# Optimization experiments

Hardware: AMD Instinct MI355X
Metric: run time of the kernel (lower is better)

Reference implementation:

```python
import jax, jax.numpy as jnp
import numpy as np

HEADS = 4
C = 128            # per-head out channels (hard-coded 128 in the module)
NEG_SLOPE_ATT = 0.2   # GATConv attention leaky_relu slope
NEG_SLOPE = 0.01      # F.leaky_relu default slope


def _diag_output_ids(num_groups, n):
    # ids = base_i + n*j + j for group i, agent j; base_i = i * n^2
    i = np.arange(num_groups)[:, None] * (n * n)
    j = np.arange(n)[None, :] * (n + 1)
    return jnp.asarray((i + j).reshape(-1))


def setup_inputs() -> dict:
    key = jax.random.key(0)
    ks = jax.random.split(key, 12)
    num_groups, n_agents = 12, 48
    N = num_groups * n_agents * n_agents      # 27648 nodes
    E = 442368
    F_in, edge_dim, hidden = 256, 16, 256
    s = 0.05
    return {
        "x": jax.random.normal(ks[0], (N, F_in), jnp.float32),
        "edge_index": jax.random.randint(ks[1], (2, E), 0, N, jnp.int32),
        "edge_attr": jax.random.normal(ks[2], (E, edge_dim), jnp.float32),
        "num_groups": num_groups,
        "agents_per_group": n_agents,
        "W": jax.random.normal(ks[3], (F_in, HEADS * C), jnp.float32) * s,
        "att_src": jax.random.normal(ks[4], (HEADS, C), jnp.float32) * s,
        "att_dst": jax.random.normal(ks[5], (HEADS, C), jnp.float32) * s,
        "W_edge": jax.random.normal(ks[6], (edge_dim, HEADS * C), jnp.float32) * s,
        "att_edge": jax.random.normal(ks[7], (HEADS, C), jnp.float32) * s,
        "bias_gat": jnp.zeros((HEADS * C,), jnp.float32),
        "fc_W": jax.random.normal(ks[8], (HEADS * C, hidden), jnp.float32) * s,
        "fc_b": jnp.zeros((hidden,), jnp.float32),
    }


def _gat_conv(x, src, dst, edge_attr_full, W, att_src, att_dst, W_edge, att_edge, bias):
    N = x.shape[0]
    h = (x @ W).reshape(N, HEADS, C)                       # [N,H,C]
    a_src = jnp.einsum('nhc,hc->nh', h, att_src)           # [N,H]
    a_dst = jnp.einsum('nhc,hc->nh', h, att_dst)
    he = (edge_attr_full @ W_edge).reshape(-1, HEADS, C)   # [E',H,C]
    a_edge = jnp.einsum('ehc,hc->eh', he, att_edge)
    logits = jax.nn.leaky_relu(a_src[src] + a_dst[dst] + a_edge, NEG_SLOPE_ATT)
    # segment softmax over incoming edges of each dst node
    m = jax.ops.segment_max(logits, dst, num_segments=N)   # [N,H]
    e = jnp.exp(logits - m[dst])
    s = jax.ops.segment_sum(e, dst, num_segments=N)
    alpha = e / (s[dst] + 1e-16)                           # [E',H]
    msg = h[src] * alpha[..., None]                        # [E',H,C]
    out = jax.ops.segment_sum(msg, dst, num_segments=N)    # [N,H,C]
    return out.reshape(N, HEADS * C) + bias


def reference(x, edge_index, edge_attr, num_groups, agents_per_group,
              W, att_src, att_dst, W_edge, att_edge, bias_gat, fc_W, fc_b):
    N = x.shape[0]
    # add self-loops (PyG default), self-loop edge_attr = mean fill
    loops = jnp.arange(N, dtype=edge_index.dtype)
    src = jnp.concatenate([edge_index[0], loops])
    dst = jnp.concatenate([edge_index[1], loops])
    ea = jnp.concatenate([edge_attr,
                          jnp.broadcast_to(edge_attr.mean(0), (N, edge_attr.shape[1]))])
    h = jax.nn.leaky_relu(
        _gat_conv(x, src, dst, ea, W, att_src, att_dst, W_edge, att_edge, bias_gat),
        NEG_SLOPE)
    ids = _diag_output_ids(num_groups, agents_per_group)
    # fc_output + leaky_relu then diagonal index-select (select first: same math)
    return jax.nn.leaky_relu(h[ids] @ fc_W + fc_b, NEG_SLOPE)
```

## Files before the change

kernel.cpp:

```cpp
#include <hip/hip_runtime.h>

#define NNODES 27648
#define NEDGES 442368
#define FIN    256
#define HC     512
#define NH     4
#define CDIM   128
#define NAG    48
#define NGRP   12
#define N2     2304
#define NOUT   576
#define CAP    128
#define EDIM   16
#define NBUCK  32

__device__ __forceinline__ float lrelu(float v, float s){ return v > 0.0f ? v : s * v; }

__device__ __forceinline__ float wsum(float v){
  #pragma unroll
  for (int off = 32; off; off >>= 1) v += __shfl_xor(v, off, 64);
  return v;
}
__device__ __forceinline__ float wmax(float v){
  #pragma unroll
  for (int off = 32; off; off >>= 1) v = fmaxf(v, __shfl_xor(v, off, 64));
  return v;
}

__global__ __launch_bounds__(256) void k_prescan(
    const float* __restrict__ W, const float* __restrict__ att_src,
    const float* __restrict__ att_dst, const float* __restrict__ W_edge,
    const float* __restrict__ att_edge,
    const int* __restrict__ ei, const float* __restrict__ ea,
    float* __restrict__ ws_, float* __restrict__ wd_, float* __restrict__ we_,
    float* __restrict__ easum32, int* __restrict__ counts,
    int2* __restrict__ slist2){
  __shared__ float4 red[16];
  int b = blockIdx.x, tid = threadIdx.x;
  if (b < NEDGES/256){
    int e = b*256 + tid;
    int dst = ei[NEDGES + e];
    int r = dst % N2;
    if (r % 49 == 0){
      int row = (dst / N2) * NAG + r / 49;
      int pos = atomicAdd(&counts[row], 1);
      if (pos < CAP) slist2[row*CAP + pos] = make_int2(ei[e], e);
    }
    const float4* p4 = (const float4*)ea + (size_t)b*1024;
    float4 acc = p4[tid];
    float4 v1 = p4[tid+256], v2 = p4[tid+512], v3 = p4[tid+768];
    acc.x += v1.x+v2.x+v3.x; acc.y += v1.y+v2.y+v3.y;
    acc.z += v1.z+v2.z+v3.z; acc.w += v1.w+v2.w+v3.w;
    #pragma unroll
    for (int off = 4; off <= 32; off <<= 1){
      acc.x += __shfl_xor(acc.x, off, 64);
      acc.y += __shfl_xor(acc.y, off, 64);
      acc.z += __shfl_xor(acc.z, off, 64);
      acc.w += __shfl_xor(acc.w, off, 64);
    }
    int lane = tid & 63, wave = tid >> 6;
    if (lane < 4) red[wave*4 + lane] = acc;
    __syncthreads();
    if (tid < 4){
      float4 t = red[tid], u = red[4+tid], v = red[8+tid], w = red[12+tid];
      t.x += u.x+v.x+w.x; t.y += u.y+v.y+w.y;
      t.z += u.z+v.z+w.z; t.w += u.w+v.w+w.w;
      float* dp = easum32 + (b & (NBUCK-1))*16 + tid*4;
      atomicAdd(dp+0, t.x); atomicAdd(dp+1, t.y);
      atomicAdd(dp+2, t.z); atomicAdd(dp+3, t.w);
    }
  } else {
    int g = (b - NEDGES/256)*256 + tid;
    if (g < 1024) {
      int f = g >> 2, h = g & 3;
      const float4* wp = (const float4*)(W + f*HC + h*CDIM);
      const float4* ap = (const float4*)(att_src + h*CDIM);
      float s = 0.f;
      #pragma unroll 8
      for (int c4 = 0; c4 < CDIM/4; c4++){
        float4 wv = wp[c4], av = ap[c4];
        s += wv.x*av.x + wv.y*av.y + wv.z*av.z + wv.w*av.w;
      }
      ws_[g] = s;
    } else if (g < 2048) {
      int gg = g - 1024; int f = gg >> 2, h = gg & 3;
      const float4* wp = (const float4*)(W + f*HC + h*CDIM);
      const float4* ap = (const float4*)(att_dst + h*CDIM);
      float s = 0.f;
      #pragma unroll 8
      for (int c4 = 0; c4 < CDIM/4; c4++){
        float4 wv = wp[c4], av = ap[c4];
        s += wv.x*av.x + wv.y*av.y + wv.z*av.z + wv.w*av.w;
      }
      wd_[gg] = s;
    } else if (g < 2112) {
      int gg = g - 2048; int d = gg >> 2, h = gg & 3;
      const float4* wp = (const float4*)(W_edge + d*HC + h*CDIM);
      const float4* ap = (const float4*)(att_edge + h*CDIM);
      float s = 0.f;
      #pragma unroll 8
      for (int c4 = 0; c4 < CDIM/4; c4++){
        float4 wv = wp[c4], av = ap[c4];
        s += wv.x*av.x + wv.y*av.y + wv.z*av.z + wv.w*av.w;
      }
      we_[gg] = s;
    }
  }
}

__global__ __launch_bounds__(256) void k_attn(const float* __restrict__ x,
    const float* __restrict__ ws_, const float* __restrict__ wd_,
    const float* __restrict__ we_, const float* __restrict__ easum32,
    const int* __restrict__ counts, const int2* __restrict__ slist2,
    const float* __restrict__ ea, float* __restrict__ z){
  __shared__ float lg[(CAP+1)*4];
  __shared__ int   srcs[CAP];
  __shared__ float adst_s[4];
  int row = blockIdx.x;
  int g = row / NAG, j = row - g*NAG;
  int dst = g*N2 + j*49;
  int tid = threadIdx.x;
  int lane = tid & 63, wave = tid >> 6;
  int k = counts[row]; if (k > CAP) k = CAP;

  float4 wev = make_float4(0.f, 0.f, 0.f, 0.f);
  if (lane < 16) wev = *(const float4*)(we_ + lane*4);

  float wsr[4][4];
  #pragma unroll
  for (int q = 0; q < 4; q++){
    float4 t = *(const float4*)(ws_ + (lane*4+q)*4);
    wsr[q][0]=t.x; wsr[q][1]=t.y; wsr[q][2]=t.z; wsr[q][3]=t.w;
  }

  for (int i = wave; i < k; i += 4){
    int2 se = slist2[row*CAP + i];
    float eav = (lane < 16) ? ea[(size_t)se.y*EDIM + lane] : 0.f;
    float4 xv = *(const float4*)(x + (size_t)se.x*FIN + lane*4);
    float p0 = xv.x*wsr[0][0] + xv.y*wsr[1][0] + xv.z*wsr[2][0] + xv.w*wsr[3][0] + eav*wev.x;
    float p1 = xv.x*wsr[0][1] + xv.y*wsr[1][1] + xv.z*wsr[2][1] + xv.w*wsr[3][1] + eav*wev.y;
    float p2 = xv.x*wsr[0][2] + xv.y*wsr[1][2] + xv.z*wsr[2][2] + xv.w*wsr[3][2] + eav*wev.z;
    float p3 = xv.x*wsr[0][3] + xv.y*wsr[1][3] + xv.z*wsr[2][3] + xv.w*wsr[3][3] + eav*wev.w;
    p0 = wsum(p0); p1 = wsum(p1); p2 = wsum(p2); p3 = wsum(p3);
    if (lane == 0){
      srcs[i] = se.x;
      lg[i*4+0] = p0; lg[i*4+1] = p1; lg[i*4+2] = p2; lg[i*4+3] = p3;
    }
  }

  if (wave == 0){
    float wdr[4][4];
    #pragma unroll
    for (int q = 0; q < 4; q++){
      float4 t = *(const float4*)(wd_ + (lane*4+q)*4);
      wdr[q][0]=t.x; wdr[q][1]=t.y; wdr[q][2]=t.z; wdr[q][3]=t.w;
    }
    float4 xv = *(const float4*)(x + (size_t)dst*FIN + lane*4);
    float pd[4], ps[4];
    #pragma unroll
    for (int h = 0; h < 4; h++){
      pd[h] = xv.x*wdr[0][h] + xv.y*wdr[1][h] + xv.z*wdr[2][h] + xv.w*wdr[3][h];
      ps[h] = xv.x*wsr[0][h] + xv.y*wsr[1][h] + xv.z*wsr[2][h] + xv.w*wsr[3][h];
    }
    float s = 0.f;
    if (lane < 16){
      #pragma unroll
      for (int bb = 0; bb < NBUCK; bb++) s += easum32[bb*16 + lane];
    }
    float md = s * (1.0f/(float)NEDGES);
    float al[4];
    al[0] = wsum(md*wev.x); al[1] = wsum(md*wev.y);
    al[2] = wsum(md*wev.z); al[3] = wsum(md*wev.w);
    #pragma unroll
    for (int h = 0; h < 4; h++){ pd[h] = wsum(pd[h]); ps[h] = wsum(ps[h]); }
    if (lane == 0){
      #pragma unroll
      for (int h = 0; h < 4; h++){
        adst_s[h] = pd[h];
        lg[k*4+h] = ps[h] + al[h];
      }
    }
  }
  __syncthreads();

  {
    int h = wave;
    float ad = adst_s[h];
    float m = -1e30f;
    for (int i = lane; i <= k; i += 64){
      float v = lrelu(lg[i*4+h] + ad, 0.2f);
      lg[i*4+h] = v;
      m = fmaxf(m, v);
    }
    m = wmax(m);
    float s = 0.f;
    for (int i = lane; i <= k; i += 64){
      float e = __expf(lg[i*4+h] - m);
      lg[i*4+h] = e;
      s += e;
    }
    s = wsum(s);
    float inv = 1.0f/(s + 1e-16f);
    for (int i = lane; i <= k; i += 64) lg[i*4+h] *= inv;
  }
  __syncthreads();

  int f = tid;
  float a0=0.f,a1=0.f,a2=0.f,a3=0.f;
  for (int i = 0; i < k; i++){
    float xv = x[(size_t)srcs[i]*FIN + f];
    a0 += lg[i*4+0]*xv; a1 += lg[i*4+1]*xv; a2 += lg[i*4+2]*xv; a3 += lg[i*4+3]*xv;
  }
  {
    float xv = x[(size_t)dst*FIN + f];
    a0 += lg[k*4+0]*xv; a1 += lg[k*4+1]*xv; a2 += lg[k*4+2]*xv; a3 += lg[k*4+3]*xv;
  }
  float* zp = z + (size_t)row*1024;
  zp[0*256+f]=a0; zp[1*256+f]=a1; zp[2*256+f]=a2; zp[3*256+f]=a3;
}

__global__ __launch_bounds__(256) void k_mlp(const float* __restrict__ z,
    const float* __restrict__ W, const float* __restrict__ bias,
    const float* __restrict__ fcW, const float* __restrict__ fcb,
    float* __restrict__ out){
  __shared__ float zs[4*1024];
  __shared__ float hs[4*512];
  int base = blockIdx.x * 4;
  int tid = threadIdx.x;
  {
    const float4* sp = (const float4*)(z + (size_t)base*1024);
    float4* dp = (float4*)zs;
    #pragma unroll
    for (int i = 0; i < 4; i++) dp[tid + i*256] = sp[tid + i*256];
  }
  __syncthreads();
  {
    int h = tid >> 6, c = tid & 63;
    int o0 = h*CDIM + c, o1 = o0 + 64;
    float a0[4] = {0,0,0,0}, a1[4] = {0,0,0,0};
    for (int k0 = 0; k0 < 256; k0 += 4){
      float w00 = W[(size_t)(k0+0)*HC + o0], w10 = W[(size_t)(k0+0)*HC + o1];
      float w01 = W[(size_t)(k0+1)*HC + o0], w11 = W[(size_t)(k0+1)*HC + o1];
      float w02 = W[(size_t)(k0+2)*HC + o0], w12 = W[(size_t)(k0+2)*HC + o1];
      float w03 = W[(size_t)(k0+3)*HC + o0], w13 = W[(size_t)(k0+3)*HC + o1];
      #pragma unroll
      for (int r = 0; r < 4; r++){
        float4 zv = *(const float4*)&zs[r*1024 + h*256 + k0];
        a0[r] += zv.x*w00 + zv.y*w01 + zv.z*w02 + zv.w*w03;
        a1[r] += zv.x*w10 + zv.y*w11 + zv.z*w12 + zv.w*w13;
      }
    }
    float b0 = bias[o0], b1 = bias[o1];
    #pragma unroll
    for (int r = 0; r < 4; r++){
      hs[r*HC + o0] = lrelu(a0[r] + b0, 0.01f);
      hs[r*HC + o1] = lrelu(a1[r] + b1, 0.01f);
    }
  }
  __syncthreads();
  {
    int j = tid;
    float acc[4] = {0,0,0,0};
    for (int q0 = 0; q0 < 512; q0 += 4){
      float f0 = fcW[(size_t)(q0+0)*256 + j];
      float f1 = fcW[(size_t)(q0+1)*256 + j];
      float f2 = fcW[(size_t)(q0+2)*256 + j];
      float f3 = fcW[(size_t)(q0+3)*256 + j];
      #pragma unroll
      for (int r = 0; r < 4; r++){
        float4 hv = *(const float4*)&hs[r*HC + q0];
        acc[r] += hv.x*f0 + hv.y*f1 + hv.z*f2 + hv.w*f3;
      }
    }
    float bj = fcb[j];
    #pragma unroll
    for (int r = 0; r < 4; r++)
      out[(size_t)(base+r)*256 + j] = lrelu(acc[r] + bj, 0.01f);
  }
}

extern "C" void kernel_launch(void* const* d_in, const int* in_sizes, int n_in,
                              void* d_out, int out_size, void* d_ws, size_t ws_size,
                              hipStream_t stream) {
  const float* x        = (const float*)d_in[0];
  const int*   ei       = (const int*)  d_in[1];
  const float* ea       = (const float*)d_in[2];
  const float* W        = (const float*)d_in[5];
  const float* att_src  = (const float*)d_in[6];
  const float* att_dst  = (const float*)d_in[7];
  const float* W_edge   = (const float*)d_in[8];
  const float* att_edge = (const float*)d_in[9];
  const float* bias     = (const float*)d_in[10];
  const float* fcW      = (const float*)d_in[11];
  const float* fcb      = (const float*)d_in[12];
  float* out = (float*)d_out;

  float* w = (float*)d_ws;
  float* ws_     = w;
  float* wd_     = w + 1024;
  float* we_     = w + 2048;
  float* easum32 = w + 2112;
  int*   counts  = (int*)(w + 2624);
  int2*  slist2  = (int2*)(w + 3200);
  float* z       = w + 150656;

  hipMemsetAsync(w + 2112, 0, (512 + 576) * sizeof(float), stream);
  k_prescan<<<NEDGES/256 + 11, 256, 0, stream>>>(
      W, att_src, att_dst, W_edge, att_edge, ei, ea,
      ws_, wd_, we_, easum32, counts, slist2);
  k_attn<<<NOUT, 256, 0, stream>>>(x, ws_, wd_, we_, easum32, counts, slist2, ea, z);
  k_mlp<<<144, 256, 0, stream>>>(z, W, bias, fcW, fcb, out);
}
```

Baseline: 166.8 us.

## Fuse prescan, attention and MLP into one cooperative persistent kernel

Replaces the memset plus three kernel launches with a single cooperative kernel of 512 blocks that runs the three phases in grid-stride loops, separated by grid-wide syncs. The goal is to remove per-launch overhead and the gaps between kernels on a workload that is short overall. The cost is grid.sync barriers, and phases that use only part of the grid (576 rows over 512 blocks, 144 MLP blocks) leave the rest idle. If the cooperative launch fails, the code falls back to the old three-kernel path.

Measured after the change: 343.5 us. +106.0%, slower.

```diff
diff --git a/kernel.cpp b/kernel.cpp
--- a/kernel.cpp
+++ b/kernel.cpp
@@ -1,4 +1,7 @@
 #include <hip/hip_runtime.h>
+#include <hip/hip_cooperative_groups.h>
+
+namespace cg = cooperative_groups;
 
 #define NNODES 27648
 #define NEDGES 442368
@@ -13,6 +16,7 @@
 #define CAP    128
 #define EDIM   16
 #define NBUCK  32
+#define GRID   512
 
 __device__ __forceinline__ float lrelu(float v, float s){ return v > 0.0f ? v : s * v; }
 
@@ -25,6 +29,244 @@
   #pragma unroll
   for (int off = 32; off; off >>= 1) v = fmaxf(v, __shfl_xor(v, off, 64));
   return v;
+}
+
+__global__ __launch_bounds__(256, 2) void k_fused(
+    const float* __restrict__ x, const int* __restrict__ ei,
+    const float* __restrict__ ea, const float* __restrict__ W,
+    const float* __restrict__ att_src, const float* __restrict__ att_dst,
+    const float* __restrict__ W_edge, const float* __restrict__ att_edge,
+    const float* __restrict__ bias, const float* __restrict__ fcW,
+    const float* __restrict__ fcb,
+    float* __restrict__ ws_, float* __restrict__ wd_, float* __restrict__ we_,
+    float* __restrict__ easum32, int* __restrict__ counts,
+    int2* __restrict__ slist2, float* __restrict__ z, float* __restrict__ out){
+  cg::grid_group grid = cg::this_grid();
+  __shared__ __align__(16) float smem[6144];
+  int b = blockIdx.x, tid = threadIdx.x;
+  int lane = tid & 63, wave = tid >> 6;
+
+  if (b == 0){
+    for (int i = tid; i < 512; i += 256) easum32[i] = 0.f;
+    for (int i = tid; i < NOUT; i += 256) counts[i] = 0;
+  }
+  grid.sync();
+
+  for (int chunk = b; chunk < 1739; chunk += GRID){
+    if (chunk < NEDGES/256){
+      int e = chunk*256 + tid;
+      int dst = ei[NEDGES + e];
+      int r = dst % N2;
+      if (r % 49 == 0){
+        int row = (dst / N2) * NAG + r / 49;
+        int pos = atomicAdd(&counts[row], 1);
+        if (pos < CAP) slist2[row*CAP + pos] = make_int2(ei[e], e);
+      }
+      const float4* p4 = (const float4*)ea + (size_t)chunk*1024;
+      float4 acc = p4[tid];
+      float4 v1 = p4[tid+256], v2 = p4[tid+512], v3 = p4[tid+768];
+      acc.x += v1.x+v2.x+v3.x; acc.y += v1.y+v2.y+v3.y;
+      acc.z += v1.z+v2.z+v3.z; acc.w += v1.w+v2.w+v3.w;
+      #pragma unroll
+      for (int off = 4; off <= 32; off <<= 1){
+        acc.x += __shfl_xor(acc.x, off, 64);
+        acc.y += __shfl_xor(acc.y, off, 64);
+        acc.z += __shfl_xor(acc.z, off, 64);
+        acc.w += __shfl_xor(acc.w, off, 64);
+      }
+      float4* red = (float4*)smem;
+      if (lane < 4) red[wave*4 + lane] = acc;
+      __syncthreads();
+      if (tid < 4){
+        float4 t = red[tid], u = red[4+tid], v = red[8+tid], w4 = red[12+tid];
+        t.x += u.x+v.x+w4.x; t.y += u.y+v.y+w4.y;
+        t.z += u.z+v.z+w4.z; t.w += u.w+v.w+w4.w;
+        float* dp = easum32 + (chunk & (NBUCK-1))*16 + tid*4;
+        atomicAdd(dp+0, t.x); atomicAdd(dp+1, t.y);
+        atomicAdd(dp+2, t.z); atomicAdd(dp+3, t.w);
+      }
+      __syncthreads();
+    } else {
+      int g = (chunk - NEDGES/256)*256 + tid;
+      const float* wmat; const float* avec; float* dstp; int gg;
+      if (g < 1024)      { gg = g;        wmat = W + (gg>>2)*HC;      avec = att_src  + (gg&3)*CDIM; dstp = ws_ + gg; }
+      else if (g < 2048) { gg = g - 1024; wmat = W + (gg>>2)*HC;      avec = att_dst  + (gg&3)*CDIM; dstp = wd_ + gg; }
+      else if (g < 2112) { gg = g - 2048; wmat = W_edge + (gg>>2)*HC; avec = att_edge + (gg&3)*CDIM; dstp = we_ + gg; }
+      else continue;
+      const float4* wp = (const float4*)(wmat + (gg&3)*CDIM);
+      const float4* ap = (const float4*)avec;
+      float s = 0.f;
+      #pragma unroll 8
+      for (int c4 = 0; c4 < CDIM/4; c4++){
+        float4 wv = wp[c4], av = ap[c4];
+        s += wv.x*av.x + wv.y*av.y + wv.z*av.z + wv.w*av.w;
+      }
+      *dstp = s;
+    }
+  }
+  grid.sync();
+
+  for (int row = b; row < NOUT; row += GRID){
+    float* lg   = smem;
+    float* adst = smem + 516;
+    int*  srcs  = (int*)(smem + 520);
+    int g = row / NAG, j = row - g*NAG;
+    int dst = g*N2 + j*49;
+    int k = counts[row]; if (k > CAP) k = CAP;
+
+    float4 wev = make_float4(0.f, 0.f, 0.f, 0.f);
+    if (lane < 16) wev = *(const float4*)(we_ + lane*4);
+
+    float wsr[4][4];
+    #pragma unroll
+    for (int q = 0; q < 4; q++){
+      float4 t = *(const float4*)(ws_ + (lane*4+q)*4);
+      wsr[q][0]=t.x; wsr[q][1]=t.y; wsr[q][2]=t.z; wsr[q][3]=t.w;
+    }
+
+    for (int i = wave; i < k; i += 4){
+      int2 se = slist2[row*CAP + i];
+      float eav = (lane < 16) ? ea[(size_t)se.y*EDIM + lane] : 0.f;
+      float4 xv = *(const float4*)(x + (size_t)se.x*FIN + lane*4);
+      float p0 = xv.x*wsr[0][0] + xv.y*wsr[1][0] + xv.z*wsr[2][0] + xv.w*wsr[3][0] + eav*wev.x;
+      float p1 = xv.x*wsr[0][1] + xv.y*wsr[1][1] + xv.z*wsr[2][1] + xv.w*wsr[3][1] + eav*wev.y;
+      float p2 = xv.x*wsr[0][2] + xv.y*wsr[1][2] + xv.z*wsr[2][2] + xv.w*wsr[3][2] + eav*wev.z;
+      float p3 = xv.x*wsr[0][3] + xv.y*wsr[1][3] + xv.z*wsr[2][3] + xv.w*wsr[3][3] + eav*wev.w;
+      p0 = wsum(p0); p1 = wsum(p1); p2 = wsum(p2); p3 = wsum(p3);
+      if (lane == 0){
+        srcs[i] = se.x;
+        lg[i*4+0] = p0; lg[i*4+1] = p1; lg[i*4+2] = p2; lg[i*4+3] = p3;
+      }
+    }
+
+    if (wave == 0){
+      float wdr[4][4];
+      #pragma unroll
+      for (int q = 0; q < 4; q++){
+        float4 t = *(const float4*)(wd_ + (lane*4+q)*4);
+        wdr[q][0]=t.x; wdr[q][1]=t.y; wdr[q][2]=t.z; wdr[q][3]=t.w;
+      }
+      float4 xv = *(const float4*)(x + (size_t)dst*FIN + lane*4);
+      float pd[4], ps[4];
+      #pragma unroll
+      for (int h = 0; h < 4; h++){
+        pd[h] = xv.x*wdr[0][h] + xv.y*wdr[1][h] + xv.z*wdr[2][h] + xv.w*wdr[3][h];
+        ps[h] = xv.x*wsr[0][h] + xv.y*wsr[1][h] + xv.z*wsr[2][h] + xv.w*wsr[3][h];
+      }
+      float s = 0.f;
+      if (lane < 16){
+        #pragma unroll
+        for (int bb = 0; bb < NBUCK; bb++) s += easum32[bb*16 + lane];
+      }
+      float md = s * (1.0f/(float)NEDGES);
+      float al[4];
+      al[0] = wsum(md*wev.x); al[1] = wsum(md*wev.y);
+      al[2] = wsum(md*wev.z); al[3] = wsum(md*wev.w);
+      #pragma unroll
+      for (int h = 0; h < 4; h++){ pd[h] = wsum(pd[h]); ps[h] = wsum(ps[h]); }
+      if (lane == 0){
+        #pragma unroll
+        for (int h = 0; h < 4; h++){
+          adst[h] = pd[h];
+          lg[k*4+h] = ps[h] + al[h];
+        }
+      }
+    }
+    __syncthreads();
+
+    {
+      int h = wave;
+      float ad = adst[h];
+      float m = -1e30f;
+      for (int i = lane; i <= k; i += 64){
+        float v = lrelu(lg[i*4+h] + ad, 0.2f);
+        lg[i*4+h] = v;
+        m = fmaxf(m, v);
+      }
+      m = wmax(m);
+      float s = 0.f;
+      for (int i = lane; i <= k; i += 64){
+        float e = __expf(lg[i*4+h] - m);
+        lg[i*4+h] = e;
+        s += e;
+      }
+      s = wsum(s);
+      float inv = 1.0f/(s + 1e-16f);
+      for (int i = lane; i <= k; i += 64) lg[i*4+h] *= inv;
+    }
+    __syncthreads();
+
+    int f = tid;
+    float a0=0.f,a1=0.f,a2=0.f,a3=0.f;
+    for (int i = 0; i < k; i++){
+      float xv = x[(size_t)srcs[i]*FIN + f];
+      a0 += lg[i*4+0]*xv; a1 += lg[i*4+1]*xv; a2 += lg[i*4+2]*xv; a3 += lg[i*4+3]*xv;
+    }
+    {
+      float xv = x[(size_t)dst*FIN + f];
+      a0 += lg[k*4+0]*xv; a1 += lg[k*4+1]*xv; a2 += lg[k*4+2]*xv; a3 += lg[k*4+3]*xv;
+    }
+    float* zp = z + (size_t)row*1024;
+    zp[0*256+f]=a0; zp[1*256+f]=a1; zp[2*256+f]=a2; zp[3*256+f]=a3;
+    __syncthreads();
+  }
+  grid.sync();
+
+  if (b < 144){
+    float* zs = smem;
+    float* hs = smem + 4096;
+    int base = b * 4;
+    {
+      const float4* sp = (const float4*)(z + (size_t)base*1024);
+      float4* dp = (float4*)zs;
+      #pragma unroll
+      for (int i = 0; i < 4; i++) dp[tid + i*256] = sp[tid + i*256];
+    }
+    __syncthreads();
+    {
+      int h = wave, c = lane;
+      int o0 = h*CDIM + c, o1 = o0 + 64;
+      float a0[4] = {0,0,0,0}, a1[4] = {0,0,0,0};
+      for (int k0 = 0; k0 < 256; k0 += 4){
+        float w00 = W[(size_t)(k0+0)*HC + o0], w10 = W[(size_t)(k0+0)*HC + o1];
+        float w01 = W[(size_t)(k0+1)*HC + o0], w11 = W[(size_t)(k0+1)*HC + o1];
+        float w02 = W[(size_t)(k0+2)*HC + o0], w12 = W[(size_t)(k0+2)*HC + o1];
+        float w03 = W[(size_t)(k0+3)*HC + o0], w13 = W[(size_t)(k0+3)*HC + o1];
+        #pragma unroll
+        for (int r = 0; r < 4; r++){
+          float4 zv = *(const float4*)&zs[r*1024 + h*256 + k0];
+          a0[r] += zv.x*w00 + zv.y*w01 + zv.z*w02 + zv.w*w03;
+          a1[r] += zv.x*w10 + zv.y*w11 + zv.z*w12 + zv.w*w13;
+        }
+      }
+      float b0 = bias[o0], b1 = bias[o1];
+      #pragma unroll
+      for (int r = 0; r < 4; r++){
+        hs[r*HC + o0] = lrelu(a0[r] + b0, 0.01f);
+        hs[r*HC + o1] = lrelu(a1[r] + b1, 0.01f);
+      }
+    }
+    __syncthreads();
+    {
+      int j = tid;
+      float acc[4] = {0,0,0,0};
+      for (int q0 = 0; q0 < 512; q0 += 4){
+        float f0 = fcW[(size_t)(q0+0)*256 + j];
+        float f1 = fcW[(size_t)(q0+1)*256 + j];
+        float f2 = fcW[(size_t)(q0+2)*256 + j];
+        float f3 = fcW[(size_t)(q0+3)*256 + j];
+        #pragma unroll
+        for (int r = 0; r < 4; r++){
+          float4 hv = *(const float4*)&hs[r*HC + q0];
+          acc[r] += hv.x*f0 + hv.y*f1 + hv.z*f2 + hv.w*f3;
+        }
+      }
+      float bj = fcb[j];
+      #pragma unroll
+      for (int r = 0; r < 4; r++)
+        out[(size_t)(base+r)*256 + j] = lrelu(acc[r] + bj, 0.01f);
+    }
+  }
 }
 
 __global__ __launch_bounds__(256) void k_prescan(
@@ -62,49 +304,29 @@
     if (lane < 4) red[wave*4 + lane] = acc;
     __syncthreads();
     if (tid < 4){
-      float4 t = red[tid], u = red[4+tid], v = red[8+tid], w = red[12+tid];
-      t.x += u.x+v.x+w.x; t.y += u.y+v.y+w.y;
-      t.z += u.z+v.z+w.z; t.w += u.w+v.w+w.w;
+      float4 t = red[tid], u = red[4+tid], v = red[8+tid], w4 = red[12+tid];
+      t.x += u.x+v.x+w4.x; t.y += u.y+v.y+w4.y;
+      t.z += u.z+v.z+w4.z; t.w += u.w+v.w+w4.w;
       float* dp = easum32 + (b & (NBUCK-1))*16 + tid*4;
       atomicAdd(dp+0, t.x); atomicAdd(dp+1, t.y);
       atomicAdd(dp+2, t.z); atomicAdd(dp+3, t.w);
     }
   } else {
     int g = (b - NEDGES/256)*256 + tid;
-    if (g < 1024) {
-      int f = g >> 2, h = g & 3;
-      const float4* wp = (const float4*)(W + f*HC + h*CDIM);
-      const float4* ap = (const float4*)(att_src + h*CDIM);
-      float s = 0.f;
-      #pragma unroll 8
-      for (int c4 = 0; c4 < CDIM/4; c4++){
-        float4 wv = wp[c4], av = ap[c4];
-        s += wv.x*av.x + wv.y*av.y + wv.z*av.z + wv.w*av.w;
-      }
-      ws_[g] = s;
-    } else if (g < 2048) {
-      int gg = g - 1024; int f = gg >> 2, h = gg & 3;
-      const float4* wp = (const float4*)(W + f*HC + h*CDIM);
-      const float4* ap = (const float4*)(att_dst + h*CDIM);
-      float s = 0.f;
-      #pragma unroll 8
-      for (int c4 = 0; c4 < CDIM/4; c4++){
-        float4 wv = wp[c4], av = ap[c4];
-        s += wv.x*av.x + wv.y*av.y + wv.z*av.z + wv.w*av.w;
-      }
-      wd_[gg] = s;
-    } else if (g < 2112) {
-      int gg = g - 2048; int d = gg >> 2, h = gg & 3;
-      const float4* wp = (const float4*)(W_edge + d*HC + h*CDIM);
-      const float4* ap = (const float4*)(att_edge + h*CDIM);
-      float s = 0.f;
-      #pragma unroll 8
-      for (int c4 = 0; c4 < CDIM/4; c4++){
-        float4 wv = wp[c4], av = ap[c4];
-        s += wv.x*av.x + wv.y*av.y + wv.z*av.z + wv.w*av.w;
-      }
-      we_[gg] = s;
-    }
+    const float* wmat; const float* avec; float* dstp; int gg;
+    if (g < 1024)      { gg = g;        wmat = W + (gg>>2)*HC;      avec = att_src  + (gg&3)*CDIM; dstp = ws_ + gg; }
+    else if (g < 2048) { gg = g - 1024; wmat = W + (gg>>2)*HC;      avec = att_dst  + (gg&3)*CDIM; dstp = wd_ + gg; }
+    else if (g < 2112) { gg = g - 2048; wmat = W_edge + (gg>>2)*HC; avec = att_edge + (gg&3)*CDIM; dstp = we_ + gg; }
+    else return;
+    const float4* wp = (const float4*)(wmat + (gg&3)*CDIM);
+    const float4* ap = (const float4*)avec;
+    float s = 0.f;
+    #pragma unroll 8
+    for (int c4 = 0; c4 < CDIM/4; c4++){
+      float4 wv = wp[c4], av = ap[c4];
+      s += wv.x*av.x + wv.y*av.y + wv.z*av.z + wv.w*av.w;
+    }
+    *dstp = s;
   }
 }
 
@@ -304,10 +526,21 @@
   int2*  slist2  = (int2*)(w + 3200);
   float* z       = w + 150656;
 
-  hipMemsetAsync(w + 2112, 0, (512 + 576) * sizeof(float), stream);
-  k_prescan<<<NEDGES/256 + 11, 256, 0, stream>>>(
-      W, att_src, att_dst, W_edge, att_edge, ei, ea,
-      ws_, wd_, we_, easum32, counts, slist2);
-  k_attn<<<NOUT, 256, 0, stream>>>(x, ws_, wd_, we_, easum32, counts, slist2, ea, z);
-  k_mlp<<<144, 256, 0, stream>>>(z, W, bias, fcW, fcb, out);
-}
+  void* args[] = {
+    (void*)&x, (void*)&ei, (void*)&ea, (void*)&W, (void*)&att_src,
+    (void*)&att_dst, (void*)&W_edge, (void*)&att_edge, (void*)&bias,
+    (void*)&fcW, (void*)&fcb,
+    (void*)&ws_, (void*)&wd_, (void*)&we_, (void*)&easum32, (void*)&counts,
+    (void*)&slist2, (void*)&z, (void*)&out};
+  hipError_t err = hipLaunchCooperativeKernel((const void*)k_fused, dim3(GRID),
+                                              dim3(256), args, 0, stream);
+  if (err != hipSuccess){
+    (void)hipGetLastError();
+    hipMemsetAsync(w + 2112, 0, (512 + 576) * sizeof(float), stream);
+    k_prescan<<<NEDGES/256 + 11, 256, 0, stream>>>(
+        W, att_src, att_dst, W_edge, att_edge, ei, ea,
+        ws_, wd_, we_, easum32, counts, slist2);
+    k_attn<<<NOUT, 256, 0, stream>>>(x, ws_, wd_, we_, easum32, counts, slist2, ea, z);
+    k_mlp<<<144, 256, 0, stream>>>(z, W, bias, fcW, fcb, out);
+  }
+}
```

## Split attention aggregation across waves with float4 gathers and paired edge loads

Applied to the files above, without the earlier changes.

The weighted aggregation in k_attn now gives each wave a subset of edges, and every lane loads float4 slices of the source rows. Partial sums from the four waves are combined through a new 16KB shared buffer. The per-thread loop over all edges with scalar loads is gone. The logit loop and the aggregation loop both handle two edges per iteration to put more loads in flight. The self-loop node is appended to srcs, and the precompute branch is consolidated without changing its behavior. The extra shared memory and reduction add a barrier and may lower occupancy.

Measured after the change: 165.8 us. About the same (-0.6%).

```diff
diff --git a/kernel.cpp b/kernel.cpp
--- a/kernel.cpp
+++ b/kernel.cpp
@@ -62,49 +62,29 @@
     if (lane < 4) red[wave*4 + lane] = acc;
     __syncthreads();
     if (tid < 4){
-      float4 t = red[tid], u = red[4+tid], v = red[8+tid], w = red[12+tid];
-      t.x += u.x+v.x+w.x; t.y += u.y+v.y+w.y;
-      t.z += u.z+v.z+w.z; t.w += u.w+v.w+w.w;
+      float4 t = red[tid], u = red[4+tid], v = red[8+tid], w4 = red[12+tid];
+      t.x += u.x+v.x+w4.x; t.y += u.y+v.y+w4.y;
+      t.z += u.z+v.z+w4.z; t.w += u.w+v.w+w4.w;
       float* dp = easum32 + (b & (NBUCK-1))*16 + tid*4;
       atomicAdd(dp+0, t.x); atomicAdd(dp+1, t.y);
       atomicAdd(dp+2, t.z); atomicAdd(dp+3, t.w);
     }
   } else {
     int g = (b - NEDGES/256)*256 + tid;
-    if (g < 1024) {
-      int f = g >> 2, h = g & 3;
-      const float4* wp = (const float4*)(W + f*HC + h*CDIM);
-      const float4* ap = (const float4*)(att_src + h*CDIM);
-      float s = 0.f;
-      #pragma unroll 8
-      for (int c4 = 0; c4 < CDIM/4; c4++){
-        float4 wv = wp[c4], av = ap[c4];
-        s += wv.x*av.x + wv.y*av.y + wv.z*av.z + wv.w*av.w;
-      }
-      ws_[g] = s;
-    } else if (g < 2048) {
-      int gg = g - 1024; int f = gg >> 2, h = gg & 3;
-      const float4* wp = (const float4*)(W + f*HC + h*CDIM);
-      const float4* ap = (const float4*)(att_dst + h*CDIM);
-      float s = 0.f;
-      #pragma unroll 8
-      for (int c4 = 0; c4 < CDIM/4; c4++){
-        float4 wv = wp[c4], av = ap[c4];
-        s += wv.x*av.x + wv.y*av.y + wv.z*av.z + wv.w*av.w;
-      }
-      wd_[gg] = s;
-    } else if (g < 2112) {
-      int gg = g - 2048; int d = gg >> 2, h = gg & 3;
-      const float4* wp = (const float4*)(W_edge + d*HC + h*CDIM);
-      const float4* ap = (const float4*)(att_edge + h*CDIM);
-      float s = 0.f;
-      #pragma unroll 8
-      for (int c4 = 0; c4 < CDIM/4; c4++){
-        float4 wv = wp[c4], av = ap[c4];
-        s += wv.x*av.x + wv.y*av.y + wv.z*av.z + wv.w*av.w;
-      }
-      we_[gg] = s;
-    }
+    const float* wmat; const float* avec; float* dstp; int gg;
+    if (g < 1024)      { gg = g;        wmat = W + (gg>>2)*HC;      avec = att_src  + (gg&3)*CDIM; dstp = ws_ + gg; }
+    else if (g < 2048) { gg = g - 1024; wmat = W + (gg>>2)*HC;      avec = att_dst  + (gg&3)*CDIM; dstp = wd_ + gg; }
+    else if (g < 2112) { gg = g - 2048; wmat = W_edge + (gg>>2)*HC; avec = att_edge + (gg&3)*CDIM; dstp = we_ + gg; }
+    else return;
+    const float4* wp = (const float4*)(wmat + (gg&3)*CDIM);
+    const float4* ap = (const float4*)avec;
+    float s = 0.f;
+    #pragma unroll 8
+    for (int c4 = 0; c4 < CDIM/4; c4++){
+      float4 wv = wp[c4], av = ap[c4];
+      s += wv.x*av.x + wv.y*av.y + wv.z*av.z + wv.w*av.w;
+    }
+    *dstp = s;
   }
 }
 
@@ -114,8 +94,9 @@
     const int* __restrict__ counts, const int2* __restrict__ slist2,
     const float* __restrict__ ea, float* __restrict__ z){
   __shared__ float lg[(CAP+1)*4];
-  __shared__ int   srcs[CAP];
   __shared__ float adst_s[4];
+  __shared__ int   srcs[CAP+1];
+  __shared__ __align__(16) float zbuf[4][4][256];
   int row = blockIdx.x;
   int g = row / NAG, j = row - g*NAG;
   int dst = g*N2 + j*49;
@@ -133,18 +114,32 @@
     wsr[q][0]=t.x; wsr[q][1]=t.y; wsr[q][2]=t.z; wsr[q][3]=t.w;
   }
 
-  for (int i = wave; i < k; i += 4){
-    int2 se = slist2[row*CAP + i];
-    float eav = (lane < 16) ? ea[(size_t)se.y*EDIM + lane] : 0.f;
-    float4 xv = *(const float4*)(x + (size_t)se.x*FIN + lane*4);
-    float p0 = xv.x*wsr[0][0] + xv.y*wsr[1][0] + xv.z*wsr[2][0] + xv.w*wsr[3][0] + eav*wev.x;
-    float p1 = xv.x*wsr[0][1] + xv.y*wsr[1][1] + xv.z*wsr[2][1] + xv.w*wsr[3][1] + eav*wev.y;
-    float p2 = xv.x*wsr[0][2] + xv.y*wsr[1][2] + xv.z*wsr[2][2] + xv.w*wsr[3][2] + eav*wev.z;
-    float p3 = xv.x*wsr[0][3] + xv.y*wsr[1][3] + xv.z*wsr[2][3] + xv.w*wsr[3][3] + eav*wev.w;
-    p0 = wsum(p0); p1 = wsum(p1); p2 = wsum(p2); p3 = wsum(p3);
+  for (int i = wave; i < k; i += 8){
+    int iB = i + 4;
+    bool hasB = iB < k;
+    int2 seA = slist2[row*CAP + i];
+    int2 seB = hasB ? slist2[row*CAP + iB] : seA;
+    float eavA = (lane < 16) ? ea[(size_t)seA.y*EDIM + lane] : 0.f;
+    float eavB = (lane < 16) ? ea[(size_t)seB.y*EDIM + lane] : 0.f;
+    float4 xvA = *(const float4*)(x + (size_t)seA.x*FIN + lane*4);
+    float4 xvB = *(const float4*)(x + (size_t)seB.x*FIN + lane*4);
+    float pA[4], pB[4];
+    #pragma unroll
+    for (int h = 0; h < 4; h++){
+      pA[h] = xvA.x*wsr[0][h] + xvA.y*wsr[1][h] + xvA.z*wsr[2][h] + xvA.w*wsr[3][h];
+      pB[h] = xvB.x*wsr[0][h] + xvB.y*wsr[1][h] + xvB.z*wsr[2][h] + xvB.w*wsr[3][h];
+    }
+    pA[0] += eavA*wev.x; pA[1] += eavA*wev.y; pA[2] += eavA*wev.z; pA[3] += eavA*wev.w;
+    pB[0] += eavB*wev.x; pB[1] += eavB*wev.y; pB[2] += eavB*wev.z; pB[3] += eavB*wev.w;
+    #pragma unroll
+    for (int h = 0; h < 4; h++){ pA[h] = wsum(pA[h]); pB[h] = wsum(pB[h]); }
     if (lane == 0){
-      srcs[i] = se.x;
-      lg[i*4+0] = p0; lg[i*4+1] = p1; lg[i*4+2] = p2; lg[i*4+3] = p3;
+      srcs[i] = seA.x;
+      lg[i*4+0]=pA[0]; lg[i*4+1]=pA[1]; lg[i*4+2]=pA[2]; lg[i*4+3]=pA[3];
+      if (hasB){
+        srcs[iB] = seB.x;
+        lg[iB*4+0]=pB[0]; lg[iB*4+1]=pB[1]; lg[iB*4+2]=pB[2]; lg[iB*4+3]=pB[3];
+      }
     }
   }
 
@@ -174,6 +169,7 @@
     #pragma unroll
     for (int h = 0; h < 4; h++){ pd[h] = wsum(pd[h]); ps[h] = wsum(ps[h]); }
     if (lane == 0){
+      srcs[k] = dst;
       #pragma unroll
       for (int h = 0; h < 4; h++){
         adst_s[h] = pd[h];
@@ -205,18 +201,38 @@
   }
   __syncthreads();
 
-  int f = tid;
-  float a0=0.f,a1=0.f,a2=0.f,a3=0.f;
-  for (int i = 0; i < k; i++){
-    float xv = x[(size_t)srcs[i]*FIN + f];
-    a0 += lg[i*4+0]*xv; a1 += lg[i*4+1]*xv; a2 += lg[i*4+2]*xv; a3 += lg[i*4+3]*xv;
-  }
-  {
-    float xv = x[(size_t)dst*FIN + f];
-    a0 += lg[k*4+0]*xv; a1 += lg[k*4+1]*xv; a2 += lg[k*4+2]*xv; a3 += lg[k*4+3]*xv;
-  }
-  float* zp = z + (size_t)row*1024;
-  zp[0*256+f]=a0; zp[1*256+f]=a1; zp[2*256+f]=a2; zp[3*256+f]=a3;
+  float4 a0 = make_float4(0,0,0,0), a1 = a0, a2 = a0, a3 = a0;
+  for (int i = wave; i <= k; i += 8){
+    int iB = i + 4;
+    bool hasB = iB <= k;
+    int sA = srcs[i];
+    int sB = hasB ? srcs[iB] : sA;
+    float4 xvA = *(const float4*)(x + (size_t)sA*FIN + lane*4);
+    float4 xvB = *(const float4*)(x + (size_t)sB*FIN + lane*4);
+    float cA0 = lg[i*4+0], cA1 = lg[i*4+1], cA2 = lg[i*4+2], cA3 = lg[i*4+3];
+    float cB0 = hasB ? lg[iB*4+0] : 0.f;
+    float cB1 = hasB ? lg[iB*4+1] : 0.f;
+    float cB2 = hasB ? lg[iB*4+2] : 0.f;
+    float cB3 = hasB ? lg[iB*4+3] : 0.f;
+    a0.x += xvA.x*cA0 + xvB.x*cB0; a0.y += xvA.y*cA0 + xvB.y*cB0;
+    a0.z += xvA.z*cA0 + xvB.z*cB0; a0.w += xvA.w*cA0 + xvB.w*cB0;
+    a1.x += xvA.x*cA1 + xvB.x*cB1; a1.y += xvA.y*cA1 + xvB.y*cB1;
+    a1.z += xvA.z*cA1 + xvB.z*cB1; a1.w += xvA.w*cA1 + xvB.w*cB1;
+    a2.x += xvA.x*cA2 + xvB.x*cB2; a2.y += xvA.y*cA2 + xvB.y*cB2;
+    a2.z += xvA.z*cA2 + xvB.z*cB2; a2.w += xvA.w*cA2 + xvB.w*cB2;
+    a3.x += xvA.x*cA3 + xvB.x*cB3; a3.y += xvA.y*cA3 + xvB.y*cB3;
+    a3.z += xvA.z*cA3 + xvB.z*cB3; a3.w += xvA.w*cA3 + xvB.w*cB3;
+  }
+  *(float4*)&zbuf[0][wave][lane*4] = a0;
+  *(float4*)&zbuf[1][wave][lane*4] = a1;
+  *(float4*)&zbuf[2][wave][lane*4] = a2;
+  *(float4*)&zbuf[3][wave][lane*4] = a3;
+  __syncthreads();
+  #pragma unroll
+  for (int h = 0; h < 4; h++){
+    float v = zbuf[h][0][tid] + zbuf[h][1][tid] + zbuf[h][2][tid] + zbuf[h][3][tid];
+    z[(size_t)row*1024 + h*256 + tid] = v;
+  }
 }
 
 __global__ __launch_bounds__(256) void k_mlp(const float* __restrict__ z,
```
